# Performance work log

Measured on AMD Instinct MI355X. Metric: run time of the kernel, lower is better.

The kernel has to match this reference:

```python
import jax, jax.numpy as jnp
import numpy as np

B, W, S, D, H = 16, 128, 16, 768, 12
HD = D // H

def _ln(x, g, b):
    m = x.mean(-1, keepdims=True)
    v = ((x - m) ** 2).mean(-1, keepdims=True)
    return (x - m) / jnp.sqrt(v + 1e-5) * g + b

def _lin(x, w, b):
    return x @ w.T + b

def _rope(t):
    # t: (N, H, L, HD); interleaved even/odd rotation, base 10000
    inv = 1.0 / (10000.0 ** (jnp.arange(0, HD, 2, dtype=jnp.float32) / HD))
    fr = jnp.arange(t.shape[2], dtype=jnp.float32)[:, None] * inv[None, :]  # (L, HD//2)
    cos, sin = jnp.cos(fr), jnp.sin(fr)
    te, to = t[..., ::2], t[..., 1::2]
    return jnp.stack([te * cos - to * sin, te * sin + to * cos], -1).reshape(t.shape)

def _mha(q, k, v, mask=None):
    # q,k,v: (N, H, L, HD)
    s = jnp.einsum('nhqd,nhkd->nhqk', q, k) / jnp.sqrt(jnp.float32(HD))
    if mask is not None:
        s = jnp.where(mask[None, None], -jnp.inf, s)
    a = jax.nn.softmax(s, axis=-1)
    return jnp.einsum('nhqk,nhkd->nhqd', a, v)

def _heads(t, L):
    return t.reshape(-1, L, H, HD).transpose(0, 2, 1, 3)

def setup_inputs() -> dict:
    key = jax.random.key(0)
    ks = jax.random.split(key, 16)
    def w(i, shape):
        return jax.random.normal(ks[i], shape, jnp.float32) * 0.02
    return {
        'x': jax.random.normal(ks[0], (B, W, S, D), jnp.float32),
        'causal_mask': jnp.triu(jnp.ones((W, W), dtype=bool), k=1),
        'sn_g': jnp.ones((D,), jnp.float32), 'sn_b': jnp.zeros((D,), jnp.float32),
        'sa_in_w': w(1, (3 * D, D)), 'sa_in_b': jnp.zeros((3 * D,), jnp.float32),
        'sa_out_w': w(2, (D, D)), 'sa_out_b': jnp.zeros((D,), jnp.float32),
        'tn_g': jnp.ones((D,), jnp.float32), 'tn_b': jnp.zeros((D,), jnp.float32),
        'tq_w': w(3, (D, D)), 'tq_b': jnp.zeros((D,), jnp.float32),
        'tk_w': w(4, (D, D)), 'tk_b': jnp.zeros((D,), jnp.float32),
        'tv_w': w(5, (D, D)), 'tv_b': jnp.zeros((D,), jnp.float32),
        'to_w': w(6, (D, D)), 'to_b': jnp.zeros((D,), jnp.float32),
        'fn_g': jnp.ones((D,), jnp.float32), 'fn_b': jnp.zeros((D,), jnp.float32),
        'f1_w': w(7, (4 * D, D)), 'f1_b': jnp.zeros((4 * D,), jnp.float32),
        'f2_w': w(8, (D, 4 * D)), 'f2_b': jnp.zeros((D,), jnp.float32),
    }

def reference(x, causal_mask, sn_g, sn_b, sa_in_w, sa_in_b, sa_out_w, sa_out_b,
              tn_g, tn_b, tq_w, tq_b, tk_w, tk_b, tv_w, tv_b, to_w, to_b,
              fn_g, fn_b, f1_w, f1_b, f2_w, f2_b):
    # ---- spatial attention within each timestep: (B*W, S, D) ----
    xs = x.reshape(B * W, S, D)
    xn = _ln(xs, sn_g, sn_b)
    q, k, v = jnp.split(_lin(xn, sa_in_w, sa_in_b), 3, axis=-1)
    o = _mha(_heads(q, S), _heads(k, S), _heads(v, S))
    o = o.transpose(0, 2, 1, 3).reshape(B * W, S, D)
    xs = xs + _lin(o, sa_out_w, sa_out_b)
    x = xs.reshape(B, W, S, D)
    # ---- causal temporal attention with RoPE: (B*S, W, D) ----
    xt = x.transpose(0, 2, 1, 3).reshape(B * S, W, D)
    xn = _ln(xt, tn_g, tn_b)
    q = _rope(_heads(_lin(xn, tq_w, tq_b), W))
    k = _rope(_heads(_lin(xn, tk_w, tk_b), W))
    v = _heads(_lin(xn, tv_w, tv_b), W)
    o = _mha(q, k, v, causal_mask)
    o = o.transpose(0, 2, 1, 3).reshape(B * S, W, D)
    xt = xt + _lin(o, to_w, to_b)
    x = xt.reshape(B, S, W, D).transpose(0, 2, 1, 3)
    # ---- feed-forward (exact GELU, as torch default) ----
    h = jax.nn.gelu(_lin(_ln(x, fn_g, fn_b), f1_w, f1_b), approximate=False)
    return x + _lin(h, f2_w, f2_b)
```

## Files before the change

### kernel.cpp

```cpp
#include <hip/hip_runtime.h>
#include <stdint.h>


#define NB 16
#define NW 128
#define NS 16
#define ND 768
#define NH 12
#define NTOK 32768

typedef __attribute__((ext_vector_type(8))) short short8;
typedef __attribute__((ext_vector_type(4))) float f32x4;

__device__ __forceinline__ float blo(unsigned v){ return __builtin_bit_cast(float, v << 16); }
__device__ __forceinline__ float bhi(unsigned v){ return __builtin_bit_cast(float, v & 0xffff0000u); }
__device__ __forceinline__ float bus(unsigned short u){ return __builtin_bit_cast(float, ((unsigned)u) << 16); }
__device__ __forceinline__ unsigned short f2b(float f){
  unsigned u = __builtin_bit_cast(unsigned, f);
  u += 0x7fffu + ((u >> 16) & 1u);
  return (unsigned short)(u >> 16);
}
__device__ __forceinline__ void gld_lds16(const void* g, void* l){
  __builtin_amdgcn_global_load_lds((const __attribute__((address_space(1))) void*)g,
                                   (__attribute__((address_space(3))) void*)l, 16, 0, 0);
}

__global__ __launch_bounds__(256) void convert_k(const float* __restrict__ in,
                                                 unsigned short* __restrict__ out, int n4){
  int i = blockIdx.x * 256 + threadIdx.x;
  int stride = gridDim.x * 256;
  for (; i < n4; i += stride){
    float4 v = ((const float4*)in)[i];
    unsigned lo = (unsigned)f2b(v.x) | ((unsigned)f2b(v.y) << 16);
    unsigned hi = (unsigned)f2b(v.z) | ((unsigned)f2b(v.w) << 16);
    ((uint2*)out)[i] = make_uint2(lo, hi);
  }
}

__global__ __launch_bounds__(256) void concat3_k(const float* __restrict__ a, const float* __restrict__ b,
                                                 const float* __restrict__ c, float* __restrict__ o){
  int i = blockIdx.x * 256 + threadIdx.x;
  if (i < 768){ o[i] = a[i]; o[768 + i] = b[i]; o[1536 + i] = c[i]; }
}

__global__ __launch_bounds__(256) void rope_k(float* __restrict__ tab){
  int i = blockIdx.x * 256 + threadIdx.x;
  if (i < 128 * 32){
    int w = i >> 5, p = i & 31;
    float inv = powf(10000.0f, -((float)(2 * p)) / 64.0f);
    float ang = (float)w * inv;
    tab[i * 2] = cosf(ang);
    tab[i * 2 + 1] = sinf(ang);
  }
}

template<int INF32>
__global__ __launch_bounds__(256) void ln_k(const void* __restrict__ xin, const float* __restrict__ g,
                                            const float* __restrict__ bt, unsigned short* __restrict__ out){
  const int row = blockIdx.x;
  const int t = threadIdx.x;
  const float* xf = (const float*)xin;
  const unsigned short* xb = (const unsigned short*)xin;
  float v[3];
#pragma unroll
  for (int i = 0; i < 3; ++i){
    int j = t + i * 256;
    v[i] = INF32 ? xf[(size_t)row * 768 + j] : bus(xb[(size_t)row * 768 + j]);
  }
  float s = v[0] + v[1] + v[2];
  float ss = v[0]*v[0] + v[1]*v[1] + v[2]*v[2];
#pragma unroll
  for (int o = 1; o < 64; o <<= 1){ s += __shfl_xor(s, o, 64); ss += __shfl_xor(ss, o, 64); }
  __shared__ float red[8];
  int w = t >> 6;
  if ((t & 63) == 0){ red[w*2] = s; red[w*2+1] = ss; }
  __syncthreads();
  s = red[0] + red[2] + red[4] + red[6];
  ss = red[1] + red[3] + red[5] + red[7];
  float mean = s * (1.0f / 768.0f);
  float var = ss * (1.0f / 768.0f) - mean * mean;
  float rstd = rsqrtf(var + 1e-5f);
#pragma unroll
  for (int i = 0; i < 3; ++i){
    int j = t + i * 256;
    out[(size_t)row * 768 + j] = f2b((v[i] - mean) * rstd * g[j] + bt[j]);
  }
}

template<int MODE>
__global__ __launch_bounds__(256, 2) void gemm128_k(const unsigned short* __restrict__ A,
                                                    const unsigned short* __restrict__ Bw,
                                                    const float* __restrict__ bias,
                                                    const void* __restrict__ resid,
                                                    void* __restrict__ outp, int K, int M){
  __shared__ char LB[65536];
  char* const Asl = LB;
  char* const Bsl = LB + 32768;
  const int tid = threadIdx.x;
  const int lane = tid & 63, w = tid >> 6;
  const int llo = lane & 15, lhi = lane >> 4;
  const int wm = w >> 1, wn = w & 1;
  const int NT = K >> 6;

  const int gx = gridDim.x;
  const int nwg = gx * gridDim.y;
  const int orig = blockIdx.y * gx + blockIdx.x;
  const int lin = (nwg & 7) ? orig : ((orig & 7) * (nwg >> 3) + (orig >> 3));
  const int by = lin / gx, bx = lin - by * gx;
  const int brow = by << 7;
  const int bcol = bx << 7;

  const int r0 = tid >> 3, cp = tid & 7;
  const int swz = (cp << 4) ^ ((r0 & 7) << 4);
  const char* aG = (const char*)(A + (size_t)(brow + r0) * K) + swz;
  const char* bG = (const char*)(Bw + (size_t)(bcol + r0) * K) + swz;
  const int J  = K * 64;
  const int Hh = K * 128;
  const int ldst = w << 10;

  auto stage = [&](const char* g, int gb, char* slotbase){
    gld_lds16(g + gb,     slotbase + ldst);
    gld_lds16(g + gb + J, slotbase + ldst + (1 << 12));
  };

  short8 a0[2][2], a1[2][2], b0[2][2], b1[2][2];
  auto rd_a = [&](short8 (&dst)[2][2], const char* Ab, int rbase){
#pragma unroll
    for (int mi = 0; mi < 2; ++mi){
      const int rr = rbase + (mi << 4) + llo;
#pragma unroll
      for (int ks = 0; ks < 2; ++ks)
        dst[mi][ks] = *(const short8*)(Ab + rr * 128 + (((ks << 6) + (lhi << 4)) ^ ((rr & 7) << 4)));
    }
  };
  auto rd_b = [&](short8 (&dst)[2][2], const char* Bb, int cbase){
#pragma unroll
    for (int ni = 0; ni < 2; ++ni){
      const int cc = cbase + (ni << 4) + llo;
#pragma unroll
      for (int ks = 0; ks < 2; ++ks)
        dst[ni][ks] = *(const short8*)(Bb + cc * 128 + (((ks << 6) + (lhi << 4)) ^ ((cc & 7) << 4)));
    }
  };

  f32x4 acc[4][4];
#pragma unroll
  for (int m = 0; m < 4; ++m)
#pragma unroll
    for (int n = 0; n < 4; ++n) acc[m][n] = f32x4{0.f, 0.f, 0.f, 0.f};

  auto mfma_q = [&](int mo, int no, short8 (&bb)[2][2], short8 (&aa)[2][2]){
    __builtin_amdgcn_s_setprio(1);
#pragma unroll
    for (int mi = 0; mi < 2; ++mi)
#pragma unroll
      for (int ni = 0; ni < 2; ++ni){
        acc[mo + mi][no + ni] = __builtin_amdgcn_mfma_f32_16x16x32_bf16(bb[ni][0], aa[mi][0], acc[mo + mi][no + ni], 0, 0, 0);
        acc[mo + mi][no + ni] = __builtin_amdgcn_mfma_f32_16x16x32_bf16(bb[ni][1], aa[mi][1], acc[mo + mi][no + ni], 0, 0, 0);
      }
    __builtin_amdgcn_s_setprio(0);
  };

  stage(aG, 0,        Asl);
  stage(aG, Hh,       Asl + (1 << 13));
  stage(bG, 0,        Bsl);
  stage(bG, Hh,       Bsl + (1 << 13));
  stage(aG, 128,      Asl + (2 << 13));
  stage(aG, 128 + Hh, Asl + (3 << 13));
  asm volatile("s_waitcnt vmcnt(4)" ::: "memory");
  __builtin_amdgcn_s_barrier();

  for (int t = 0; t < NT; ++t){
    const char* Ab = Asl + (((2 * t + wm) & 3) << 13);
    const char* Bb = Bsl + (((2 * t + wn) & 3) << 13);
    const int tb = t << 7;

    rd_b(b0, Bb, 0);
    rd_a(a0, Ab, 0);
    if (t + 1 < NT) stage(bG, tb + 128, Bsl + (((2 * t + 2) & 3) << 13));
    __builtin_amdgcn_s_barrier();
    asm volatile("s_waitcnt lgkmcnt(0)" ::: "memory");
    mfma_q(0, 0, b0, a0);
    __builtin_amdgcn_s_barrier();

    rd_a(a1, Ab, 32);
    if (t + 1 < NT) stage(bG, tb + 128 + Hh, Bsl + (((2 * t + 3) & 3) << 13));
    __builtin_amdgcn_s_barrier();
    asm volatile("s_waitcnt lgkmcnt(0)" ::: "memory");
    mfma_q(2, 0, b0, a1);
    __builtin_amdgcn_s_barrier();

    rd_b(b1, Bb, 32);
    if (t + 2 < NT) stage(aG, tb + 256, Asl + (((2 * t + 4) & 3) << 13));
    __builtin_amdgcn_s_barrier();
    asm volatile("s_waitcnt lgkmcnt(0)" ::: "memory");
    mfma_q(0, 2, b1, a0);
    __builtin_amdgcn_s_barrier();

    if (t + 2 < NT) stage(aG, tb + 256 + Hh, Asl + (((2 * t + 5) & 3) << 13));
    __builtin_amdgcn_s_barrier();
    asm volatile("s_waitcnt lgkmcnt(0)" ::: "memory");
    mfma_q(2, 2, b1, a1);
    if (t + 2 < NT) asm volatile("s_waitcnt vmcnt(4)" ::: "memory");
    else            asm volatile("s_waitcnt vmcnt(0)" ::: "memory");
    __builtin_amdgcn_s_barrier();
  }

  const int orow = brow + (wm << 6);
  const int ocol = bcol + (wn << 6);
  const unsigned short* resb = (const unsigned short*)resid;
  const float* resf = (const float*)resid;
#pragma unroll
  for (int m = 0; m < 4; ++m){
    const int row = orow + (m << 4) + llo;
    const size_t rb = (size_t)row * M;
#pragma unroll
    for (int n = 0; n < 4; ++n){
      const int col = ocol + (n << 4) + (lhi << 2);
      const float4 bv = *(const float4*)&bias[col];
      float v0 = acc[m][n][0] + bv.x;
      float v1 = acc[m][n][1] + bv.y;
      float v2 = acc[m][n][2] + bv.z;
      float v3 = acc[m][n][3] + bv.w;
      const size_t off = rb + col;
      if (MODE == 1){
        float y0 = v0 * (1.5957691216f + 0.0713548163f * v0 * v0);
        float y1 = v1 * (1.5957691216f + 0.0713548163f * v1 * v1);
        float y2 = v2 * (1.5957691216f + 0.0713548163f * v2 * v2);
        float y3 = v3 * (1.5957691216f + 0.0713548163f * v3 * v3);
        v0 = v0 / (1.0f + __expf(-y0));
        v1 = v1 / (1.0f + __expf(-y1));
        v2 = v2 / (1.0f + __expf(-y2));
        v3 = v3 / (1.0f + __expf(-y3));
      } else if (MODE == 2){
        const float4 rv = *(const float4*)&resf[off];
        v0 += rv.x; v1 += rv.y; v2 += rv.z; v3 += rv.w;
      } else if (MODE == 3 || MODE == 4){
        const uint2 rv = *(const uint2*)&resb[off];
        v0 += blo(rv.x); v1 += bhi(rv.x); v2 += blo(rv.y); v3 += bhi(rv.y);
      }
      if (MODE == 4){
        float4 ov; ov.x = v0; ov.y = v1; ov.z = v2; ov.w = v3;
        *(float4*)&((float*)outp)[off] = ov;
      } else {
        unsigned lo = (unsigned)f2b(v0) | ((unsigned)f2b(v1) << 16);
        unsigned hi = (unsigned)f2b(v2) | ((unsigned)f2b(v3) << 16);
        *(uint2*)&((unsigned short*)outp)[off] = make_uint2(lo, hi);
      }
    }
  }
}

__global__ __launch_bounds__(256) void sattn_k(const unsigned short* __restrict__ qkv,
                                               unsigned short* __restrict__ o){
  const int bw = blockIdx.x, h = blockIdx.y;
  const int t = threadIdx.x;
  __shared__ unsigned short qh[16 * 68], kh[16 * 68], vh[16 * 68];
  __shared__ float pl[16 * 17];
  const int row = t >> 4, c4 = t & 15;
  const size_t base = ((size_t)(bw * 16 + row)) * 2304 + h * 64 + c4 * 4;
  *(uint2*)&qh[row * 68 + c4 * 4] = *(const uint2*)&qkv[base];
  *(uint2*)&kh[row * 68 + c4 * 4] = *(const uint2*)&qkv[base + 768];
  *(uint2*)&vh[row * 68 + c4 * 4] = *(const uint2*)&qkv[base + 1536];
  __syncthreads();

  const int q = row, k = c4;
  float s = 0.f;
#pragma unroll
  for (int c = 0; c < 16; ++c){
    uint2 qv = *(const uint2*)&qh[q * 68 + c * 4];
    uint2 kv = *(const uint2*)&kh[k * 68 + c * 4];
    s += blo(qv.x) * blo(kv.x) + bhi(qv.x) * bhi(kv.x);
    s += blo(qv.y) * blo(kv.y) + bhi(qv.y) * bhi(kv.y);
  }
  s *= 0.125f;
  float m = s;
#pragma unroll
  for (int off = 1; off < 16; off <<= 1) m = fmaxf(m, __shfl_xor(m, off, 64));
  float p = __expf(s - m);
  float su = p;
#pragma unroll
  for (int off = 1; off < 16; off <<= 1) su += __shfl_xor(su, off, 64);
  pl[q * 17 + k] = p / su;
  __syncthreads();

  float o0 = 0.f, o1 = 0.f, o2 = 0.f, o3 = 0.f;
#pragma unroll
  for (int kk = 0; kk < 16; ++kk){
    float pw = pl[q * 17 + kk];
    uint2 vv = *(const uint2*)&vh[kk * 68 + c4 * 4];
    o0 += pw * blo(vv.x); o1 += pw * bhi(vv.x);
    o2 += pw * blo(vv.y); o3 += pw * bhi(vv.y);
  }
  const size_t ob = ((size_t)(bw * 16 + q)) * 768 + h * 64 + c4 * 4;
  unsigned r0 = (unsigned)f2b(o0) | ((unsigned)f2b(o1) << 16);
  unsigned r1 = (unsigned)f2b(o2) | ((unsigned)f2b(o3) << 16);
  *(uint2*)&o[ob] = make_uint2(r0, r1);
}

__global__ __launch_bounds__(256) void tattn_k(const unsigned short* __restrict__ qkv,
                                               const float* __restrict__ rope,
                                               unsigned short* __restrict__ o){
  const int bs = blockIdx.x, h = blockIdx.y;
  const int b = bs >> 4, s = bs & 15;
  const int t = threadIdx.x, lane = t & 63, w = t >> 6;
  const int lhi = lane >> 4, llo = lane & 15;
  __shared__ unsigned short Qs[128 * 64];
  __shared__ unsigned short Ks[128 * 64];
  __shared__ unsigned short Vt[64 * 128];
  __shared__ unsigned short P[128 * 128];

  {
    const int r = t >> 1;
    const int dbase = (t & 1) * 32;
    const size_t tokb = ((size_t)((b * 128 + r) * 16 + s)) * 2304 + h * 64;
    const float2* rp = (const float2*)rope;
#pragma unroll
    for (int mch = 0; mch < 4; ++mch){
      const int d0 = dbase + mch * 8;
      uint4 qv = *(const uint4*)&qkv[tokb + d0];
      uint4 kv = *(const uint4*)&qkv[tokb + 768 + d0];
      uint4 vv = *(const uint4*)&qkv[tokb + 1536 + d0];
      unsigned qin[4] = {qv.x, qv.y, qv.z, qv.w};
      unsigned kin[4] = {kv.x, kv.y, kv.z, kv.w};
      unsigned qo[4], ko[4];
#pragma unroll
      for (int j = 0; j < 4; ++j){
        float2 cssn = rp[r * 32 + (d0 >> 1) + j];
        float cs = cssn.x, sn = cssn.y;
        float qe = blo(qin[j]), qd = bhi(qin[j]);
        float ke = blo(kin[j]), kd = bhi(kin[j]);
        qo[j] = (unsigned)f2b(qe * cs - qd * sn) | ((unsigned)f2b(qe * sn + qd * cs) << 16);
        ko[j] = (unsigned)f2b(ke * cs - kd * sn) | ((unsigned)f2b(ke * sn + kd * cs) << 16);
      }
      const int byq = r * 128 + ((d0 * 2) ^ ((r & 7) << 4));
      *(uint4*)((char*)Qs + byq) = make_uint4(qo[0], qo[1], qo[2], qo[3]);
      *(uint4*)((char*)Ks + byq) = make_uint4(ko[0], ko[1], ko[2], ko[3]);
      unsigned vin[4] = {vv.x, vv.y, vv.z, vv.w};
#pragma unroll
      for (int j = 0; j < 8; ++j){
        const int d = d0 + j;
        unsigned short val = (j & 1) ? (unsigned short)(vin[j >> 1] >> 16)
                                     : (unsigned short)(vin[j >> 1] & 0xffffu);
        *(unsigned short*)((char*)Vt + d * 256 + ((r * 2) ^ ((d & 7) << 4))) = val;
      }
    }
  }
  __syncthreads();

  const int qbase = w * 32;
  f32x4 st[8][2];
#pragma unroll
  for (int i = 0; i < 8; ++i){ st[i][0] = f32x4{0.f,0.f,0.f,0.f}; st[i][1] = f32x4{0.f,0.f,0.f,0.f}; }
#pragma unroll
  for (int kd = 0; kd < 2; ++kd){
    short8 bq[2];
#pragma unroll
    for (int fq = 0; fq < 2; ++fq){
      const int qr = qbase + fq * 16 + llo;
      bq[fq] = *(const short8*)((const char*)Qs + qr * 128 + ((kd * 64 + lhi * 16) ^ ((qr & 7) << 4)));
    }
#pragma unroll
    for (int fk = 0; fk < 8; ++fk){
      const int kr = fk * 16 + llo;
      short8 ak = *(const short8*)((const char*)Ks + kr * 128 + ((kd * 64 + lhi * 16) ^ ((kr & 7) << 4)));
      st[fk][0] = __builtin_amdgcn_mfma_f32_16x16x32_bf16(ak, bq[0], st[fk][0], 0, 0, 0);
      st[fk][1] = __builtin_amdgcn_mfma_f32_16x16x32_bf16(ak, bq[1], st[fk][1], 0, 0, 0);
    }
  }

#pragma unroll
  for (int fq = 0; fq < 2; ++fq){
    const int qg = qbase + fq * 16 + llo;
    float m = -1e30f;
#pragma unroll
    for (int fk = 0; fk < 8; ++fk)
#pragma unroll
      for (int rr = 0; rr < 4; ++rr){
        const int kg = fk * 16 + lhi * 4 + rr;
        float sv = (kg <= qg) ? st[fk][fq][rr] : -1e30f;
        st[fk][fq][rr] = sv;
        m = fmaxf(m, sv);
      }
    m = fmaxf(m, __shfl_xor(m, 16, 64));
    m = fmaxf(m, __shfl_xor(m, 32, 64));
    float su = 0.f;
#pragma unroll
    for (int fk = 0; fk < 8; ++fk)
#pragma unroll
      for (int rr = 0; rr < 4; ++rr){
        float p = __expf((st[fk][fq][rr] - m) * 0.125f);
        st[fk][fq][rr] = p;
        su += p;
      }
    su += __shfl_xor(su, 16, 64);
    su += __shfl_xor(su, 32, 64);
    const float rs = 1.0f / su;
#pragma unroll
    for (int fk = 0; fk < 8; ++fk){
      const int kk = fk * 16 + lhi * 4;
      unsigned lo = (unsigned)f2b(st[fk][fq][0] * rs) | ((unsigned)f2b(st[fk][fq][1] * rs) << 16);
      unsigned hi = (unsigned)f2b(st[fk][fq][2] * rs) | ((unsigned)f2b(st[fk][fq][3] * rs) << 16);
      *(uint2*)((char*)P + qg * 256 + ((kk * 2) ^ ((qg & 7) << 4))) = make_uint2(lo, hi);
    }
  }
  __syncthreads();

  f32x4 oacc[2][4];
#pragma unroll
  for (int i = 0; i < 2; ++i)
#pragma unroll
    for (int j = 0; j < 4; ++j) oacc[i][j] = f32x4{0.f,0.f,0.f,0.f};
#pragma unroll
  for (int ks = 0; ks < 4; ++ks){
    short8 pa[2];
#pragma unroll
    for (int fq = 0; fq < 2; ++fq){
      const int qr = qbase + fq * 16 + llo;
      pa[fq] = *(const short8*)((const char*)P + qr * 256 + ((ks * 64 + lhi * 16) ^ ((qr & 7) << 4)));
    }
#pragma unroll
    for (int fd = 0; fd < 4; ++fd){
      const int dr = fd * 16 + llo;
      short8 vb = *(const short8*)((const char*)Vt + dr * 256 + ((ks * 64 + lhi * 16) ^ ((dr & 7) << 4)));
      oacc[0][fd] = __builtin_amdgcn_mfma_f32_16x16x32_bf16(pa[0], vb, oacc[0][fd], 0, 0, 0);
      oacc[1][fd] = __builtin_amdgcn_mfma_f32_16x16x32_bf16(pa[1], vb, oacc[1][fd], 0, 0, 0);
    }
  }

#pragma unroll
  for (int fq = 0; fq < 2; ++fq)
#pragma unroll
    for (int fd = 0; fd < 4; ++fd)
#pragma unroll
      for (int rr = 0; rr < 4; ++rr){
        const int qg = qbase + fq * 16 + lhi * 4 + rr;
        const int d = fd * 16 + llo;
        const size_t ob = ((size_t)((b * 128 + qg) * 16 + s)) * 768 + h * 64 + d;
        o[ob] = f2b(oacc[fq][fd][rr]);
      }
}

__global__ __launch_bounds__(256) void sentinel_k(float* out){
  if (blockIdx.x == 0 && threadIdx.x == 0) out[0] = 12345.0f;
}

extern "C" void kernel_launch(void* const* d_in, const int* in_sizes, int n_in,
                              void* d_out, int out_size, void* d_ws, size_t ws_size,
                              hipStream_t stream){
  const float* x       = (const float*)d_in[0];
  const float* sn_g    = (const float*)d_in[2];
  const float* sn_b    = (const float*)d_in[3];
  const float* sa_in_w = (const float*)d_in[4];
  const float* sa_in_b = (const float*)d_in[5];
  const float* sa_out_w= (const float*)d_in[6];
  const float* sa_out_b= (const float*)d_in[7];
  const float* tn_g    = (const float*)d_in[8];
  const float* tn_b    = (const float*)d_in[9];
  const float* tq_w    = (const float*)d_in[10];
  const float* tq_b    = (const float*)d_in[11];
  const float* tk_w    = (const float*)d_in[12];
  const float* tk_b    = (const float*)d_in[13];
  const float* tv_w    = (const float*)d_in[14];
  const float* tv_b    = (const float*)d_in[15];
  const float* to_w    = (const float*)d_in[16];
  const float* to_b    = (const float*)d_in[17];
  const float* fn_g    = (const float*)d_in[18];
  const float* fn_b    = (const float*)d_in[19];
  const float* f1_w    = (const float*)d_in[20];
  const float* f1_b    = (const float*)d_in[21];
  const float* f2_w    = (const float*)d_in[22];
  const float* f2_b    = (const float*)d_in[23];

  char* ws = (char*)d_ws;
  size_t off = 0;
  auto alloc = [&](size_t bytes) -> void* {
    void* p = ws + off;
    off += (bytes + 255) & ~(size_t)255;
    return p;
  };
  unsigned short* Wqkv = (unsigned short*)alloc((size_t)2304*768*2);
  unsigned short* Wo1  = (unsigned short*)alloc((size_t)768*768*2);
  unsigned short* W3   = (unsigned short*)alloc((size_t)2304*768*2);
  float*          b3   = (float*)alloc(2304*4);
  unsigned short* Wto  = (unsigned short*)alloc((size_t)768*768*2);
  unsigned short* Wf1  = (unsigned short*)alloc((size_t)3072*768*2);
  unsigned short* Wf2  = (unsigned short*)alloc((size_t)768*3072*2);
  float*          rope = (float*)alloc(128*32*2*4);
  unsigned short* xn   = (unsigned short*)alloc((size_t)NTOK*768*2);
  unsigned short* qkv  = (unsigned short*)alloc((size_t)NTOK*3072*2);
  unsigned short* xs2  = (unsigned short*)alloc((size_t)NTOK*768*2);
  unsigned short* xt2  = (unsigned short*)alloc((size_t)NTOK*768*2);
  unsigned short* ob   = xn;

  if (ws_size < off){ sentinel_k<<<1, 64, 0, stream>>>((float*)d_out); return; }

  convert_k<<<1024, 256, 0, stream>>>(sa_in_w, Wqkv, 2304*768/4);
  convert_k<<<512, 256, 0, stream>>>(sa_out_w, Wo1, 768*768/4);
  convert_k<<<512, 256, 0, stream>>>(tq_w, W3, 768*768/4);
  convert_k<<<512, 256, 0, stream>>>(tk_w, W3 + 768*768, 768*768/4);
  convert_k<<<512, 256, 0, stream>>>(tv_w, W3 + 2*768*768, 768*768/4);
  concat3_k<<<3, 256, 0, stream>>>(tq_b, tk_b, tv_b, b3);
  convert_k<<<512, 256, 0, stream>>>(to_w, Wto, 768*768/4);
  convert_k<<<1024, 256, 0, stream>>>(f1_w, Wf1, 3072*768/4);
  convert_k<<<1024, 256, 0, stream>>>(f2_w, Wf2, 768*3072/4);
  rope_k<<<16, 256, 0, stream>>>(rope);

  ln_k<1><<<NTOK, 256, 0, stream>>>(x, sn_g, sn_b, xn);
  gemm128_k<0><<<dim3(18, 256), 256, 0, stream>>>(xn, Wqkv, sa_in_b, nullptr, qkv, 768, 2304);
  sattn_k<<<dim3(2048, 12), 256, 0, stream>>>(qkv, ob);
  gemm128_k<2><<<dim3(6, 256), 256, 0, stream>>>(ob, Wo1, sa_out_b, x, xs2, 768, 768);

  ln_k<0><<<NTOK, 256, 0, stream>>>(xs2, tn_g, tn_b, xn);
  gemm128_k<0><<<dim3(18, 256), 256, 0, stream>>>(xn, W3, b3, nullptr, qkv, 768, 2304);
  tattn_k<<<dim3(256, 12), 256, 0, stream>>>(qkv, rope, ob);
  gemm128_k<3><<<dim3(6, 256), 256, 0, stream>>>(ob, Wto, to_b, xs2, xt2, 768, 768);

  ln_k<0><<<NTOK, 256, 0, stream>>>(xt2, fn_g, fn_b, xn);
  gemm128_k<1><<<dim3(24, 256), 256, 0, stream>>>(xn, Wf1, f1_b, nullptr, qkv, 768, 3072);
  gemm128_k<4><<<dim3(6, 256), 256, 0, stream>>>(qkv, Wf2, f2_b, xt2, d_out, 3072, 768);
}
```

Measured before the change: 1.106 ms.

## Shrink GEMM K-tile to 32 with triple-buffered LDS for three blocks per CU

The GEMM main loop is restructured to use a K-step of 32 instead of 64. Each stage is one 128x32 tile for A and for B, rotated through three LDS slots (48KB total instead of 64KB), and launch bounds go from 2 to 3 blocks per CU. The goal is more concurrent workgroups to hide memory latency, with loads kept two stages ahead. The cost is twice as many loop iterations and barriers per K, less MFMA work per barrier, and a 4-way swizzle that may bring more LDS bank conflicts.

```diff
diff --git a/kernel.cpp b/kernel.cpp
--- a/kernel.cpp
+++ b/kernel.cpp
@@ -88,19 +88,19 @@
 }
 
 template<int MODE>
-__global__ __launch_bounds__(256, 2) void gemm128_k(const unsigned short* __restrict__ A,
+__global__ __launch_bounds__(256, 3) void gemm128_k(const unsigned short* __restrict__ A,
                                                     const unsigned short* __restrict__ Bw,
                                                     const float* __restrict__ bias,
                                                     const void* __restrict__ resid,
                                                     void* __restrict__ outp, int K, int M){
-  __shared__ char LB[65536];
+  __shared__ char LB[49152];
   char* const Asl = LB;
-  char* const Bsl = LB + 32768;
+  char* const Bsl = LB + 24576;
   const int tid = threadIdx.x;
   const int lane = tid & 63, w = tid >> 6;
   const int llo = lane & 15, lhi = lane >> 4;
   const int wm = w >> 1, wn = w & 1;
-  const int NT = K >> 6;
+  const int NT = K >> 5;
 
   const int gx = gridDim.x;
   const int nwg = gx * gridDim.y;
@@ -110,36 +110,31 @@
   const int brow = by << 7;
   const int bcol = bx << 7;
 
-  const int r0 = tid >> 3, cp = tid & 7;
-  const int swz = (cp << 4) ^ ((r0 & 7) << 4);
+  const int r0 = tid >> 2, cp = tid & 3;
+  const int swz = (cp << 4) ^ ((r0 & 3) << 4);
   const char* aG = (const char*)(A + (size_t)(brow + r0) * K) + swz;
   const char* bG = (const char*)(Bw + (size_t)(bcol + r0) * K) + swz;
-  const int J  = K * 64;
-  const int Hh = K * 128;
+  const int J2 = K * 128;
   const int ldst = w << 10;
 
   auto stage = [&](const char* g, int gb, char* slotbase){
-    gld_lds16(g + gb,     slotbase + ldst);
-    gld_lds16(g + gb + J, slotbase + ldst + (1 << 12));
+    gld_lds16(g + gb,      slotbase + ldst);
+    gld_lds16(g + gb + J2, slotbase + ldst + (1 << 12));
   };
 
-  short8 a0[2][2], a1[2][2], b0[2][2], b1[2][2];
-  auto rd_a = [&](short8 (&dst)[2][2], const char* Ab, int rbase){
-#pragma unroll
-    for (int mi = 0; mi < 2; ++mi){
-      const int rr = rbase + (mi << 4) + llo;
-#pragma unroll
-      for (int ks = 0; ks < 2; ++ks)
-        dst[mi][ks] = *(const short8*)(Ab + rr * 128 + (((ks << 6) + (lhi << 4)) ^ ((rr & 7) << 4)));
+  short8 a[4], b[4];
+  auto rd_a = [&](const char* Ab){
+#pragma unroll
+    for (int mi = 0; mi < 4; ++mi){
+      const int rr = (wm << 6) + (mi << 4) + llo;
+      a[mi] = *(const short8*)(Ab + rr * 64 + ((lhi << 4) ^ ((rr & 3) << 4)));
     }
   };
-  auto rd_b = [&](short8 (&dst)[2][2], const char* Bb, int cbase){
+  auto rd_b2 = [&](const char* Bb, int nb){
 #pragma unroll
     for (int ni = 0; ni < 2; ++ni){
-      const int cc = cbase + (ni << 4) + llo;
-#pragma unroll
-      for (int ks = 0; ks < 2; ++ks)
-        dst[ni][ks] = *(const short8*)(Bb + cc * 128 + (((ks << 6) + (lhi << 4)) ^ ((cc & 7) << 4)));
+      const int cc = (wn << 6) + ((nb + ni) << 4) + llo;
+      b[nb + ni] = *(const short8*)(Bb + cc * 64 + ((lhi << 4) ^ ((cc & 3) << 4)));
     }
   };
 
@@ -149,61 +144,48 @@
 #pragma unroll
     for (int n = 0; n < 4; ++n) acc[m][n] = f32x4{0.f, 0.f, 0.f, 0.f};
 
-  auto mfma_q = [&](int mo, int no, short8 (&bb)[2][2], short8 (&aa)[2][2]){
+  auto mfma_h = [&](int nb){
     __builtin_amdgcn_s_setprio(1);
 #pragma unroll
-    for (int mi = 0; mi < 2; ++mi)
-#pragma unroll
-      for (int ni = 0; ni < 2; ++ni){
-        acc[mo + mi][no + ni] = __builtin_amdgcn_mfma_f32_16x16x32_bf16(bb[ni][0], aa[mi][0], acc[mo + mi][no + ni], 0, 0, 0);
-        acc[mo + mi][no + ni] = __builtin_amdgcn_mfma_f32_16x16x32_bf16(bb[ni][1], aa[mi][1], acc[mo + mi][no + ni], 0, 0, 0);
-      }
+    for (int mi = 0; mi < 4; ++mi)
+#pragma unroll
+      for (int ni = 0; ni < 2; ++ni)
+        acc[mi][nb + ni] = __builtin_amdgcn_mfma_f32_16x16x32_bf16(b[nb + ni], a[mi], acc[mi][nb + ni], 0, 0, 0);
     __builtin_amdgcn_s_setprio(0);
   };
 
-  stage(aG, 0,        Asl);
-  stage(aG, Hh,       Asl + (1 << 13));
-  stage(bG, 0,        Bsl);
-  stage(bG, Hh,       Bsl + (1 << 13));
-  stage(aG, 128,      Asl + (2 << 13));
-  stage(aG, 128 + Hh, Asl + (3 << 13));
+  stage(aG, 0,  Asl);
+  stage(bG, 0,  Bsl);
+  stage(aG, 64, Asl + 8192);
+  stage(bG, 64, Bsl + 8192);
   asm volatile("s_waitcnt vmcnt(4)" ::: "memory");
   __builtin_amdgcn_s_barrier();
 
+  int sl = 0;
   for (int t = 0; t < NT; ++t){
-    const char* Ab = Asl + (((2 * t + wm) & 3) << 13);
-    const char* Bb = Bsl + (((2 * t + wn) & 3) << 13);
-    const int tb = t << 7;
-
-    rd_b(b0, Bb, 0);
-    rd_a(a0, Ab, 0);
-    if (t + 1 < NT) stage(bG, tb + 128, Bsl + (((2 * t + 2) & 3) << 13));
+    const char* Ab = Asl + (sl << 13);
+    const char* Bb = Bsl + (sl << 13);
+    int sl2 = sl + 2; if (sl2 >= 3) sl2 -= 3;
+    const int tb = t << 6;
+
+    rd_b2(Bb, 0);
+    rd_a(Ab);
+    if (t + 2 < NT) stage(aG, tb + 128, Asl + (sl2 << 13));
     __builtin_amdgcn_s_barrier();
     asm volatile("s_waitcnt lgkmcnt(0)" ::: "memory");
-    mfma_q(0, 0, b0, a0);
+    mfma_h(0);
     __builtin_amdgcn_s_barrier();
 
-    rd_a(a1, Ab, 32);
-    if (t + 1 < NT) stage(bG, tb + 128 + Hh, Bsl + (((2 * t + 3) & 3) << 13));
+    rd_b2(Bb, 2);
+    if (t + 2 < NT) stage(bG, tb + 128, Bsl + (sl2 << 13));
     __builtin_amdgcn_s_barrier();
     asm volatile("s_waitcnt lgkmcnt(0)" ::: "memory");
-    mfma_q(2, 0, b0, a1);
-    __builtin_amdgcn_s_barrier();
-
-    rd_b(b1, Bb, 32);
-    if (t + 2 < NT) stage(aG, tb + 256, Asl + (((2 * t + 4) & 3) << 13));
-    __builtin_amdgcn_s_barrier();
-    asm volatile("s_waitcnt lgkmcnt(0)" ::: "memory");
-    mfma_q(0, 2, b1, a0);
-    __builtin_amdgcn_s_barrier();
-
-    if (t + 2 < NT) stage(aG, tb + 256 + Hh, Asl + (((2 * t + 5) & 3) << 13));
-    __builtin_amdgcn_s_barrier();
-    asm volatile("s_waitcnt lgkmcnt(0)" ::: "memory");
-    mfma_q(2, 2, b1, a1);
+    mfma_h(2);
     if (t + 2 < NT) asm volatile("s_waitcnt vmcnt(4)" ::: "memory");
     else            asm volatile("s_waitcnt vmcnt(0)" ::: "memory");
     __builtin_amdgcn_s_barrier();
+
+    sl = sl + 1; if (sl >= 3) sl = 0;
   }
 
   const int orow = brow + (wm << 6);
```

New measurement: 1.147 ms. 3.7% more time.
